# Kernel tuning notes

Measured on AMD Instinct MI355X. Metric: run time of the kernel, lower is better.

The kernel has to match this reference:

```python
import jax, jax.numpy as jnp
import numpy as np

HIDDEN = 512


def setup_inputs() -> dict:
    key = jax.random.key(0)
    ks = jax.random.split(key, 5)
    S, B, I, H = 256, 128, 1024, HIDDEN
    scale_ih = 1.0 / np.sqrt(H)
    return {
        "x": jax.random.normal(ks[0], (S, B, I), dtype=jnp.float32),
        "w_ih": jax.random.normal(ks[1], (4 * H, I), dtype=jnp.float32) * scale_ih,
        "w_hh": jax.random.normal(ks[2], (4 * H, H), dtype=jnp.float32) * scale_ih,
        "b_ih": jax.random.normal(ks[3], (4 * H,), dtype=jnp.float32) * scale_ih,
        "b_hh": jax.random.normal(ks[4], (4 * H,), dtype=jnp.float32) * scale_ih,
    }


def reference(x, w_ih, w_hh, b_ih, b_hh):
    # x: [S, B, I]. LSTMCell with PyTorch gate order (i, f, g, o).
    S, B, _ = x.shape
    H = HIDDEN
    bias = b_ih + b_hh  # fuse both biases

    def step(carry, xt):
        h, c = carry
        gates = xt @ w_ih.T + h @ w_hh.T + bias  # [B, 4H]
        i, f, g, o = jnp.split(gates, 4, axis=-1)
        i = jax.nn.sigmoid(i)
        f = jax.nn.sigmoid(f)
        g = jnp.tanh(g)
        o = jax.nn.sigmoid(o)
        c = f * c + i * g
        h = o * jnp.tanh(c)
        # original code's h[arange(B)] / c[arange(B)] is an identity gather: no-op
        return (h, c), None

    h0 = jnp.zeros((B, H), dtype=x.dtype)
    c0 = jnp.zeros((B, H), dtype=x.dtype)
    (h, c), _ = jax.lax.scan(step, (h0, c0), x)
    return h.sum()
```

## Files before the change

### kernel.cpp

```cpp
#include <hip/hip_runtime.h>

typedef __attribute__((ext_vector_type(8))) short short8;
typedef __attribute__((ext_vector_type(4))) float f32x4;

#define S_LEN 256
#define BATCH 128
#define IN_DIM 1024
#define HID 512
#define G4 2048

#define SENT 0xFFFFFFFFu

__device__ __forceinline__ unsigned short f32_bf16(float f) {
  unsigned int u = __float_as_uint(f);
  u = (u + 0x7FFFu + ((u >> 16) & 1u)) >> 16;
  return (unsigned short)u;
}
__device__ __forceinline__ float bf16_f32(unsigned short h) {
  return __uint_as_float(((unsigned int)h) << 16);
}
__device__ __forceinline__ float sigm(float x) { return 1.0f / (1.0f + __expf(-x)); }
__device__ __forceinline__ float tanh_fast(float x) {
  return 1.0f - 2.0f / (__expf(2.0f * x) + 1.0f);
}

__global__ void cvt_bf16(const float* __restrict__ src, unsigned short* __restrict__ dst, int n) {
  int i = (blockIdx.x * blockDim.x + threadIdx.x) * 4;
  if (i >= n) return;
  float4 v = *(const float4*)(src + i);
  ushort4 o;
  o.x = f32_bf16(v.x); o.y = f32_bf16(v.y); o.z = f32_bf16(v.z); o.w = f32_bf16(v.w);
  *(ushort4*)(dst + i) = o;
}

__global__ void init_all(const float* __restrict__ b_ih, const float* __restrict__ b_hh,
                         float* __restrict__ bias, uint4* __restrict__ hring4) {
  int i = blockIdx.x * blockDim.x + threadIdx.x;
  if (i < G4) bias[i] = b_ih[i] + b_hh[i];
  const int SLOT4 = BATCH * HID / 8;
  const int TOT4 = 257 * SLOT4;
  const uint4 z = make_uint4(0u, 0u, 0u, 0u);
  const uint4 sN = make_uint4(SENT, SENT, SENT, SENT);
  for (int k = i; k < TOT4; k += gridDim.x * blockDim.x)
    hring4[k] = (k < SLOT4) ? z : sN;
}

__device__ __forceinline__ void gl_lds16(const void* g, void* l) {
  __builtin_amdgcn_global_load_lds(
      (const __attribute__((address_space(1))) unsigned int*)g,
      (__attribute__((address_space(3))) unsigned int*)l, 16, 0, 0);
}

template <int C_F32>
__global__ __launch_bounds__(256) void gemm_bias(
    const unsigned short* __restrict__ A,
    const unsigned short* __restrict__ Bw,
    const float* __restrict__ bias,
    void* __restrict__ Cout) {
  __shared__ __align__(16) unsigned short As[128 * 32];
  __shared__ __align__(16) unsigned short Bs[128 * 32];
  const int tid = threadIdx.x;
  const int w = tid >> 6, l = tid & 63;
  const int wm = w & 1, wn = w >> 1;
  const int nt = blockIdx.x & 15, mt = blockIdx.x >> 4;

  f32x4 acc[4][4];
#pragma unroll
  for (int i = 0; i < 4; i++)
#pragma unroll
    for (int j = 0; j < 4; j++) acc[i][j] = f32x4{0.f, 0.f, 0.f, 0.f};

  for (int k0 = 0; k0 < 1024; k0 += 32) {
    __syncthreads();
#pragma unroll
    for (int jj = 0; jj < 2; jj++) {
      int cid = (w * 2 + jj) * 64 + l;
      int row = cid >> 2, kc = cid & 3;
      const unsigned short* ga = A + (size_t)(mt * 128 + row) * 1024 + k0 + kc * 8;
      gl_lds16(ga, As + (w * 2 + jj) * 512);
      const unsigned short* gb = Bw + (size_t)(nt * 128 + row) * 1024 + k0 + kc * 8;
      gl_lds16(gb, Bs + (w * 2 + jj) * 512);
    }
    __syncthreads();
    short8 a[4], b[4];
#pragma unroll
    for (int i = 0; i < 4; i++)
      a[i] = *(const short8*)&As[(wm * 64 + i * 16 + (l & 15)) * 32 + (l >> 4) * 8];
#pragma unroll
    for (int j = 0; j < 4; j++)
      b[j] = *(const short8*)&Bs[(wn * 64 + j * 16 + (l & 15)) * 32 + (l >> 4) * 8];
#pragma unroll
    for (int i = 0; i < 4; i++)
#pragma unroll
      for (int j = 0; j < 4; j++)
        acc[i][j] = __builtin_amdgcn_mfma_f32_16x16x32_bf16(a[i], b[j], acc[i][j], 0, 0, 0);
  }
#pragma unroll
  for (int j = 0; j < 4; j++) {
    int cg = nt * 128 + wn * 64 + j * 16 + (l & 15);
    float bv = bias[cg];
#pragma unroll
    for (int i = 0; i < 4; i++) {
      int rbase = mt * 128 + wm * 64 + i * 16 + (l >> 4) * 4;
#pragma unroll
      for (int r = 0; r < 4; r++) {
        float v = acc[i][j][r] + bv;
        if (C_F32)
          ((float*)Cout)[(size_t)(rbase + r) * 2048 + cg] = v;
        else
          ((unsigned short*)Cout)[(size_t)(rbase + r) * 2048 + cg] = f32_bf16(v);
      }
    }
  }
}

__global__ __launch_bounds__(256, 1) void lstm_rec(
    const unsigned short* __restrict__ whh,
    const void* __restrict__ gx,
    int gx_f32,
    unsigned* __restrict__ hring) {
  __shared__ __align__(16) unsigned short Hs[2][16][520];
  __shared__ __align__(16) float Gt[16][132];

  const int tid = threadIdx.x;
  const int w = tid >> 6, l = tid & 63;
  const int m = blockIdx.x & 7;
  const int s = blockIdx.x >> 3;

  short8 bw[16][2];
#pragma unroll
  for (int u = 0; u < 2; u++) {
    int n = (2 * w + u) * 16 + (l & 15);
    int jn = n >> 2, g = n & 3;
    int R = g * 512 + s * 32 + jn;
    const unsigned short* base = whh + (size_t)R * 512 + ((l >> 4) * 8);
#pragma unroll
    for (int kk = 0; kk < 16; kk++) bw[kk][u] = *(const short8*)(base + kk * 32);
  }

  const int b = l & 15;
  const int p = 4 * w + (l >> 4);
  const int gb = m * 16 + b;
  const int colg = s * 32 + 2 * p;
  float c0 = 0.f, c1 = 0.f;

  const float* gxf = (const float*)gx;
  const unsigned short* gxb = (const unsigned short*)gx;
  const int SLOTW = BATCH * HID / 2;
  const unsigned long long* hull = (const unsigned long long*)hring;
  const int SLOTQ = BATCH * HID / 4;

  const int skc = tid & 127;
  const int srow = tid >> 7;

  for (int t = 0; t < S_LEN; t++) {
    float2 pg[4];
    {
      size_t base = (size_t)(t * BATCH + gb) * G4 + colg;
      if (gx_f32) {
#pragma unroll
        for (int g = 0; g < 4; g++) pg[g] = *(const float2*)(gxf + base + (size_t)g * 512);
      } else {
#pragma unroll
        for (int g = 0; g < 4; g++) {
          unsigned u = *(const unsigned*)(gxb + base + (size_t)g * 512);
          pg[g].x = bf16_f32((unsigned short)(u & 0xFFFFu));
          pg[g].y = bf16_f32((unsigned short)(u >> 16));
        }
      }
    }

    const unsigned long long* src = hull + (size_t)t * SLOTQ;
    unsigned long long v[8];
#pragma unroll
    for (int it = 0; it < 8; it++)
      v[it] = __hip_atomic_load(&src[(size_t)(m * 16 + it * 2 + srow) * 128 + skc],
                                __ATOMIC_RELAXED, __HIP_MEMORY_SCOPE_AGENT);
    for (;;) {
      int bad = 0;
#pragma unroll
      for (int it = 0; it < 8; it++)
        bad |= (((unsigned)v[it] == SENT) | ((unsigned)(v[it] >> 32) == SENT)) << it;
      if (!bad) break;
#pragma unroll
      for (int it = 0; it < 8; it++)
        if ((bad >> it) & 1)
          v[it] = __hip_atomic_load(&src[(size_t)(m * 16 + it * 2 + srow) * 128 + skc],
                                    __ATOMIC_RELAXED, __HIP_MEMORY_SCOPE_AGENT);
    }
    const int buf = t & 1;
#pragma unroll
    for (int it = 0; it < 8; it++)
      *(unsigned long long*)&Hs[buf][it * 2 + srow][skc * 4] = v[it];
    __syncthreads();

    f32x4 acc0 = f32x4{0.f, 0.f, 0.f, 0.f};
    f32x4 acc1 = f32x4{0.f, 0.f, 0.f, 0.f};
#pragma unroll
    for (int kk = 0; kk < 16; kk++) {
      short8 a = *(const short8*)&Hs[buf][l & 15][kk * 32 + (l >> 4) * 8];
      acc0 = __builtin_amdgcn_mfma_f32_16x16x32_bf16(a, bw[kk][0], acc0, 0, 0, 0);
      acc1 = __builtin_amdgcn_mfma_f32_16x16x32_bf16(a, bw[kk][1], acc1, 0, 0, 0);
    }

#pragma unroll
    for (int r = 0; r < 4; r++) {
      Gt[(l >> 4) * 4 + r][(2 * w + 0) * 16 + (l & 15)] = acc0[r];
      Gt[(l >> 4) * 4 + r][(2 * w + 1) * 16 + (l & 15)] = acc1[r];
    }

    float4 g0 = *(const float4*)&Gt[b][8 * p];
    float4 g1 = *(const float4*)&Gt[b][8 * p + 4];
    float i0 = sigm(g0.x + pg[0].x), f0 = sigm(g0.y + pg[1].x);
    float gg0 = tanh_fast(g0.z + pg[2].x), o0 = sigm(g0.w + pg[3].x);
    c0 = f0 * c0 + i0 * gg0;
    float h0 = o0 * tanh_fast(c0);
    float i1 = sigm(g1.x + pg[0].y), f1 = sigm(g1.y + pg[1].y);
    float gg1 = tanh_fast(g1.z + pg[2].y), o1 = sigm(g1.w + pg[3].y);
    c1 = f1 * c1 + i1 * gg1;
    float h1 = o1 * tanh_fast(c1);
    unsigned hp = (unsigned)f32_bf16(h0) | ((unsigned)f32_bf16(h1) << 16);

    __hip_atomic_store(&hring[(size_t)(t + 1) * SLOTW + gb * 256 + s * 16 + p], hp,
                       __ATOMIC_RELAXED, __HIP_MEMORY_SCOPE_AGENT);
  }
}

__global__ void reduce_sum(const unsigned short* __restrict__ h, float* __restrict__ out) {
  __shared__ float red[256];
  int tid = threadIdx.x;
  float s = 0.f;
  for (int i = tid * 8; i < BATCH * HID; i += 256 * 8) {
    uint4 v = *(const uint4*)(h + i);
    unsigned int q[4] = {v.x, v.y, v.z, v.w};
#pragma unroll
    for (int k = 0; k < 4; k++) {
      s += bf16_f32((unsigned short)(q[k] & 0xFFFFu));
      s += bf16_f32((unsigned short)(q[k] >> 16));
    }
  }
  red[tid] = s;
  __syncthreads();
  for (int off = 128; off > 0; off >>= 1) {
    if (tid < off) red[tid] += red[tid + off];
    __syncthreads();
  }
  if (tid == 0) out[0] = red[0];
}

extern "C" void kernel_launch(void* const* d_in, const int* in_sizes, int n_in,
                              void* d_out, int out_size, void* d_ws, size_t ws_size,
                              hipStream_t stream) {
  const float* x = (const float*)d_in[0];
  const float* w_ih = (const float*)d_in[1];
  const float* w_hh = (const float*)d_in[2];
  const float* b_ih = (const float*)d_in[3];
  const float* b_hh = (const float*)d_in[4];

  char* ws = (char*)d_ws;
  unsigned short* x_bf = (unsigned short*)(ws);
  unsigned short* wih_bf = (unsigned short*)(ws + 67108864);
  unsigned short* whh_bf = (unsigned short*)(ws + 71303168);
  float* bias = (float*)(ws + 73400320);
  unsigned* hring = (unsigned*)(ws + 73408512);
  void* gx = (void*)(ws + 107094016);

  const size_t need_f32 = 107094016ull + (size_t)S_LEN * BATCH * G4 * 4;
  int gx_f32 = (ws_size >= need_f32) ? 1 : 0;

  cvt_bf16<<<(33554432 / 4 + 255) / 256, 256, 0, stream>>>(x, x_bf, 33554432);
  cvt_bf16<<<(2097152 / 4 + 255) / 256, 256, 0, stream>>>(w_ih, wih_bf, 2097152);
  cvt_bf16<<<(1048576 / 4 + 255) / 256, 256, 0, stream>>>(w_hh, whh_bf, 1048576);
  init_all<<<256, 256, 0, stream>>>(b_ih, b_hh, bias, (uint4*)hring);

  if (gx_f32)
    gemm_bias<1><<<4096, 256, 0, stream>>>(x_bf, wih_bf, bias, gx);
  else
    gemm_bias<0><<<4096, 256, 0, stream>>>(x_bf, wih_bf, bias, gx);

  void* args[] = {(void*)&whh_bf, (void*)&gx, (void*)&gx_f32, (void*)&hring};
  hipLaunchCooperativeKernel((const void*)lstm_rec, dim3(128), dim3(256), args, 0, stream);

  reduce_sum<<<1, 256, 0, stream>>>((const unsigned short*)(hring + 256 * (BATCH * HID / 2)),
                                    (float*)d_out);
}
```

Before: 1.275 ms.

## Prefetch next-step hidden state and gate inputs; write own h slice locally

The recurrent LSTM loop now issues the loads for step t+1's hidden-state ring slice and precomputed input gates right after the barrier, so they overlap with the MFMA and gate math of step t. Each block also writes its own freshly computed h slice straight into the next LDS buffer and skips polling global memory for that portion. The aim is to hide the global-memory and inter-block spin latency on the serial critical path. In exchange it adds register pressure from the extra prefetch buffers, and a speculative early load may still see sentinels and need repolling.

```diff
diff --git a/kernel.cpp b/kernel.cpp
--- a/kernel.cpp
+++ b/kernel.cpp
@@ -152,47 +152,75 @@
 
   const int skc = tid & 127;
   const int srow = tid >> 7;
+  const bool selfst = (((tid >> 3) & 15) == s);
+
+  unsigned long long v[8];
+#pragma unroll
+  for (int it = 0; it < 8; it++)
+    v[it] = __hip_atomic_load(&hull[(size_t)(m * 16 + it * 2 + srow) * 128 + skc],
+                              __ATOMIC_RELAXED, __HIP_MEMORY_SCOPE_AGENT);
+  float2 pg[4];
+  {
+    size_t base0 = (size_t)gb * G4 + colg;
+    if (gx_f32) {
+#pragma unroll
+      for (int g = 0; g < 4; g++) pg[g] = *(const float2*)(gxf + base0 + (size_t)g * 512);
+    } else {
+#pragma unroll
+      for (int g = 0; g < 4; g++) {
+        unsigned u = *(const unsigned*)(gxb + base0 + (size_t)g * 512);
+        pg[g].x = bf16_f32((unsigned short)(u & 0xFFFFu));
+        pg[g].y = bf16_f32((unsigned short)(u >> 16));
+      }
+    }
+  }
 
   for (int t = 0; t < S_LEN; t++) {
-    float2 pg[4];
-    {
-      size_t base = (size_t)(t * BATCH + gb) * G4 + colg;
+    const int buf = t & 1;
+    const unsigned long long* src = hull + (size_t)t * SLOTQ;
+
+    if (!(selfst && t > 0)) {
+      for (;;) {
+        int bad = 0;
+#pragma unroll
+        for (int it = 0; it < 8; it++)
+          bad |= (((unsigned)v[it] == SENT) | ((unsigned)(v[it] >> 32) == SENT)) << it;
+        if (!bad) break;
+#pragma unroll
+        for (int it = 0; it < 8; it++)
+          if ((bad >> it) & 1)
+            v[it] = __hip_atomic_load(&src[(size_t)(m * 16 + it * 2 + srow) * 128 + skc],
+                                      __ATOMIC_RELAXED, __HIP_MEMORY_SCOPE_AGENT);
+      }
+#pragma unroll
+      for (int it = 0; it < 8; it++)
+        *(unsigned long long*)&Hs[buf][it * 2 + srow][skc * 4] = v[it];
+    }
+    __syncthreads();
+
+    unsigned long long vn[8];
+    float2 pgn[4];
+    if (t + 1 < S_LEN) {
+      if (!selfst) {
+        const unsigned long long* srcn = hull + (size_t)(t + 1) * SLOTQ;
+#pragma unroll
+        for (int it = 0; it < 8; it++)
+          vn[it] = __hip_atomic_load(&srcn[(size_t)(m * 16 + it * 2 + srow) * 128 + skc],
+                                     __ATOMIC_RELAXED, __HIP_MEMORY_SCOPE_AGENT);
+      }
+      size_t basen = (size_t)((t + 1) * BATCH + gb) * G4 + colg;
       if (gx_f32) {
 #pragma unroll
-        for (int g = 0; g < 4; g++) pg[g] = *(const float2*)(gxf + base + (size_t)g * 512);
+        for (int g = 0; g < 4; g++) pgn[g] = *(const float2*)(gxf + basen + (size_t)g * 512);
       } else {
 #pragma unroll
         for (int g = 0; g < 4; g++) {
-          unsigned u = *(const unsigned*)(gxb + base + (size_t)g * 512);
-          pg[g].x = bf16_f32((unsigned short)(u & 0xFFFFu));
-          pg[g].y = bf16_f32((unsigned short)(u >> 16));
+          unsigned u = *(const unsigned*)(gxb + basen + (size_t)g * 512);
+          pgn[g].x = bf16_f32((unsigned short)(u & 0xFFFFu));
+          pgn[g].y = bf16_f32((unsigned short)(u >> 16));
         }
       }
     }
-
-    const unsigned long long* src = hull + (size_t)t * SLOTQ;
-    unsigned long long v[8];
-#pragma unroll
-    for (int it = 0; it < 8; it++)
-      v[it] = __hip_atomic_load(&src[(size_t)(m * 16 + it * 2 + srow) * 128 + skc],
-                                __ATOMIC_RELAXED, __HIP_MEMORY_SCOPE_AGENT);
-    for (;;) {
-      int bad = 0;
-#pragma unroll
-      for (int it = 0; it < 8; it++)
-        bad |= (((unsigned)v[it] == SENT) | ((unsigned)(v[it] >> 32) == SENT)) << it;
-      if (!bad) break;
-#pragma unroll
-      for (int it = 0; it < 8; it++)
-        if ((bad >> it) & 1)
-          v[it] = __hip_atomic_load(&src[(size_t)(m * 16 + it * 2 + srow) * 128 + skc],
-                                    __ATOMIC_RELAXED, __HIP_MEMORY_SCOPE_AGENT);
-    }
-    const int buf = t & 1;
-#pragma unroll
-    for (int it = 0; it < 8; it++)
-      *(unsigned long long*)&Hs[buf][it * 2 + srow][skc * 4] = v[it];
-    __syncthreads();
 
     f32x4 acc0 = f32x4{0.f, 0.f, 0.f, 0.f};
     f32x4 acc1 = f32x4{0.f, 0.f, 0.f, 0.f};
@@ -223,6 +251,12 @@
 
     __hip_atomic_store(&hring[(size_t)(t + 1) * SLOTW + gb * 256 + s * 16 + p], hp,
                        __ATOMIC_RELAXED, __HIP_MEMORY_SCOPE_AGENT);
+    *(unsigned*)&Hs[buf ^ 1][b][colg] = hp;
+
+#pragma unroll
+    for (int it = 0; it < 8; it++) v[it] = vn[it];
+#pragma unroll
+    for (int g = 0; g < 4; g++) pg[g] = pgn[g];
   }
 }
 
```

Result: faster. 1.204 ms (-5.5%).
